# Kernel tuning notes

Measured on AMD Instinct MI355X. Metric: run time of the kernel, lower is better.

The kernel has to match this reference:

```python
import jax, jax.numpy as jnp
import numpy as np

B = 8          # batch (number of ragged segments)
N = 4096       # trigram sets per sequence (uniform segments)
K = 3          # trigram token ids per set
V = 100000     # vocab_size
H = 1024       # hidden_size
SEQ = 2048     # sequence_length / seq_len


def setup_inputs() -> dict:
    key = jax.random.key(0)
    k1, k2 = jax.random.split(key)
    trigram_token_ids = jax.random.randint(k1, (B * N, K), 0, V, dtype=jnp.int32)
    # each position covered by exactly 2 trigram sets; per-segment positions start at 0
    pos_one = (jnp.arange(N, dtype=jnp.int32) // 2)  # [N], values 0..SEQ-1
    trigram_set_position_ids = jnp.tile(pos_one, B)  # [B*N]
    starts = jnp.arange(B, dtype=jnp.int32) * N
    trigram_token_ids_offsets = jnp.stack([starts, starts + N], axis=1)  # [B,2]
    std = (2.0 / (5.0 * H)) ** 0.5  # pythia init
    W = jax.random.normal(k2, (V, H), dtype=jnp.float32) * std
    return {
        "trigram_set_position_ids": trigram_set_position_ids,
        "trigram_token_ids": trigram_token_ids,
        "trigram_token_ids_offsets": trigram_token_ids_offsets,
        "seq_len": SEQ,
        "W": W,
    }


def reference(trigram_set_position_ids, trigram_token_ids, trigram_token_ids_offsets, seq_len, W):
    # Uniform ragged segments: reshape flat arrays to [B, n, ...] using offsets count.
    b = trigram_token_ids_offsets.shape[0]
    total, k = trigram_token_ids.shape
    n = total // b
    tok = trigram_token_ids.reshape(b, n, k)          # [B, n, K]
    pos = trigram_set_position_ids.reshape(b, n)      # [B, n]
    # gather + mean-aggregate over the K trigram ids of each set
    emb = W[tok].mean(axis=2)                         # [B, n, H]

    def scatter_one(p, e):
        # index_add scatter of set embeddings onto sequence positions
        s = jax.ops.segment_sum(e, p, num_segments=seq_len)                       # [seq, H]
        c = jax.ops.segment_sum(jnp.ones((n,), e.dtype), p, num_segments=seq_len)  # [seq]
        c = jnp.where(c == 0, jnp.ones((), e.dtype), c)  # counts of 0 -> 1 (normalization guard)
        return s / c[:, None]

    return jax.vmap(scatter_one)(pos, emb)            # [B, seq, H]
```

## Files before the change

### kernel.cpp

```cpp
#include <hip/hip_runtime.h>

#define CAP 8
#define RPB 16

__global__ void build_map_kernel(const int* __restrict__ pos_ids,
                                 const int* __restrict__ tok,
                                 int total, int n_per, int seq, int K,
                                 int* __restrict__ counts,
                                 int* __restrict__ toktab) {
    int i = blockIdx.x * blockDim.x + threadIdx.x;
    if (i >= total) return;
    int b = i / n_per;
    int p = pos_ids[i];
    if ((unsigned)p >= (unsigned)seq) return;
    int bp = b * seq + p;
    int c = atomicAdd(&counts[bp], 1);
    if (c < CAP) {
        int* dst = toktab + (size_t)bp * (CAP * K) + c * K;
        for (int k = 0; k < K; ++k) dst[k] = tok[i * K + k];
    }
}

#define SORT2(a, b) { int _lo = min(a, b); int _hi = max(a, b); a = _lo; b = _hi; }

__global__ void sort_rows_kernel(const int* __restrict__ counts,
                                 int* __restrict__ toktab,
                                 int nrows, int K) {
    int i = blockIdx.x * blockDim.x + threadIdx.x;
    if (i >= nrows) return;
    int cnt = counts[i];
    int ce = cnt < CAP ? cnt : CAP;
    int n = ce * K;
    int stride = CAP * K;
    int* row = toktab + (size_t)i * stride;
    if (n == 6) {
        int t0=row[0],t1=row[1],t2=row[2],t3=row[3],t4=row[4],t5=row[5];
        SORT2(t1,t2) SORT2(t4,t5) SORT2(t0,t2) SORT2(t3,t5)
        SORT2(t0,t1) SORT2(t3,t4) SORT2(t1,t4) SORT2(t0,t3)
        SORT2(t2,t5) SORT2(t1,t3) SORT2(t2,t4) SORT2(t2,t3)
        row[0]=t0;row[1]=t1;row[2]=t2;row[3]=t3;row[4]=t4;row[5]=t5;
    } else if (n > 1) {
        int tmp[CAP * 8];
        if (n > CAP * 8) n = CAP * 8;
        for (int j = 0; j < n; ++j) tmp[j] = row[j];
        for (int a = 1; a < n; ++a) {
            int v = tmp[a]; int q = a - 1;
            while (q >= 0 && tmp[q] > v) { tmp[q + 1] = tmp[q]; --q; }
            tmp[q + 1] = v;
        }
        for (int j = 0; j < n; ++j) row[j] = tmp[j];
    }
}

__global__ __launch_bounds__(256, 4)
void gather_out_kernel(const float* __restrict__ W,
                       const int* __restrict__ counts,
                       const int* __restrict__ toktab,
                       float* __restrict__ out,
                       int K, int H, int nrows) {
    int r0 = blockIdx.x * RPB;
    int h = threadIdx.x * 4;
    int stride = CAP * K;

    int cnt[RPB];
    bool allsix = true;
    #pragma unroll
    for (int r = 0; r < RPB; ++r) {
        int row = r0 + r;
        cnt[r] = (row < nrows) ? counts[row] : 0;
        int ce = cnt[r] < CAP ? cnt[r] : CAP;
        if (ce * K != 6) allsix = false;
    }

    float4 acc[RPB];
    #pragma unroll
    for (int r = 0; r < RPB; ++r) acc[r] = make_float4(0.f, 0.f, 0.f, 0.f);

    if (allsix) {
        #pragma unroll
        for (int j = 0; j < 6; ++j) {
            #pragma unroll
            for (int r = 0; r < RPB; ++r) {
                int t = toktab[(size_t)(r0 + r) * stride + j];
                const float4 v = *(const float4*)(W + (size_t)t * H + h);
                acc[r].x += v.x; acc[r].y += v.y;
                acc[r].z += v.z; acc[r].w += v.w;
            }
        }
    } else {
        #pragma unroll
        for (int r = 0; r < RPB; ++r) {
            int ce = cnt[r] < CAP ? cnt[r] : CAP;
            int ntok = ce * K;
            for (int j = 0; j < ntok; ++j) {
                int t = toktab[(size_t)(r0 + r) * stride + j];
                const float4 v = *(const float4*)(W + (size_t)t * H + h);
                acc[r].x += v.x; acc[r].y += v.y;
                acc[r].z += v.z; acc[r].w += v.w;
            }
        }
    }

    #pragma unroll
    for (int r = 0; r < RPB; ++r) {
        int row = r0 + r;
        if (row >= nrows) continue;
        float denom = (float)K * (float)(cnt[r] > 0 ? cnt[r] : 1);
        float s = 1.0f / denom;
        float* op = out + (size_t)row * H + h;
        __builtin_nontemporal_store(acc[r].x * s, op + 0);
        __builtin_nontemporal_store(acc[r].y * s, op + 1);
        __builtin_nontemporal_store(acc[r].z * s, op + 2);
        __builtin_nontemporal_store(acc[r].w * s, op + 3);
    }
}

extern "C" void kernel_launch(void* const* d_in, const int* in_sizes, int n_in,
                              void* d_out, int out_size, void* d_ws, size_t ws_size,
                              hipStream_t stream) {
    const int*   pos_ids = (const int*)d_in[0];
    const int*   tok     = (const int*)d_in[1];
    const float* W       = (const float*)d_in[4];
    float*       out     = (float*)d_out;

    const int B     = in_sizes[2] / 2;
    const int total = in_sizes[0];
    const int n_per = total / B;
    const int K     = in_sizes[1] / total;
    const int H     = 1024;
    const int seq   = out_size / (B * H);
    const int nrows = B * seq;

    int* counts = (int*)d_ws;
    int* toktab = counts + (size_t)nrows;

    hipMemsetAsync(counts, 0, (size_t)nrows * sizeof(int), stream);

    int bthreads = 256;
    int bblocks  = (total + bthreads - 1) / bthreads;
    build_map_kernel<<<bblocks, bthreads, 0, stream>>>(pos_ids, tok, total,
                                                       n_per, seq, K,
                                                       counts, toktab);

    int sblocks = (nrows + bthreads - 1) / bthreads;
    sort_rows_kernel<<<sblocks, bthreads, 0, stream>>>(counts, toktab,
                                                       nrows, K);

    int gblocks = (nrows + RPB - 1) / RPB;
    gather_out_kernel<<<gblocks, H / 4, 0, stream>>>(W, counts, toktab,
                                                     out, K, H, nrows);
}
```

Measured before the change: 88.82 us.

## Fold row sort into gather and split vocab gathers into barrier-synced phases

Removes the separate sort kernel by sorting each row's token ids in shared memory inside the gather kernel. The gather is then split into two vocab-range phases separated by a grid-wide soft barrier, so that all blocks touch the same half of W at once and it is more likely to stay in cache. The barrier gives up after a spin limit, so correctness does not depend on it, but blocks that finish early may sleep-wait. It also adds a per-token range check and shared-memory indexing inside the hot loop.

After: 244.6 us. 2.75x slower.

```diff
diff --git a/kernel.cpp b/kernel.cpp
--- a/kernel.cpp
+++ b/kernel.cpp
@@ -1,7 +1,10 @@
 #include <hip/hip_runtime.h>
 
 #define CAP 8
+#define MAXT (CAP * 3)
 #define RPB 16
+#define NPHASE 2
+#define SPIN_LIMIT 2000
 
 __global__ void build_map_kernel(const int* __restrict__ pos_ids,
                                  const int* __restrict__ tok,
@@ -23,89 +26,92 @@
 
 #define SORT2(a, b) { int _lo = min(a, b); int _hi = max(a, b); a = _lo; b = _hi; }
 
-__global__ void sort_rows_kernel(const int* __restrict__ counts,
-                                 int* __restrict__ toktab,
-                                 int nrows, int K) {
-    int i = blockIdx.x * blockDim.x + threadIdx.x;
-    if (i >= nrows) return;
-    int cnt = counts[i];
-    int ce = cnt < CAP ? cnt : CAP;
-    int n = ce * K;
-    int stride = CAP * K;
-    int* row = toktab + (size_t)i * stride;
-    if (n == 6) {
-        int t0=row[0],t1=row[1],t2=row[2],t3=row[3],t4=row[4],t5=row[5];
-        SORT2(t1,t2) SORT2(t4,t5) SORT2(t0,t2) SORT2(t3,t5)
-        SORT2(t0,t1) SORT2(t3,t4) SORT2(t1,t4) SORT2(t0,t3)
-        SORT2(t2,t5) SORT2(t1,t3) SORT2(t2,t4) SORT2(t2,t3)
-        row[0]=t0;row[1]=t1;row[2]=t2;row[3]=t3;row[4]=t4;row[5]=t5;
-    } else if (n > 1) {
-        int tmp[CAP * 8];
-        if (n > CAP * 8) n = CAP * 8;
-        for (int j = 0; j < n; ++j) tmp[j] = row[j];
-        for (int a = 1; a < n; ++a) {
-            int v = tmp[a]; int q = a - 1;
-            while (q >= 0 && tmp[q] > v) { tmp[q + 1] = tmp[q]; --q; }
-            tmp[q + 1] = v;
+__device__ void soft_barrier(int* ctr, int target) {
+    __syncthreads();
+    if (threadIdx.x == 0) {
+        __hip_atomic_fetch_add(ctr, 1, __ATOMIC_ACQ_REL, __HIP_MEMORY_SCOPE_AGENT);
+        int spins = 0;
+        while (__hip_atomic_load(ctr, __ATOMIC_ACQUIRE,
+                                 __HIP_MEMORY_SCOPE_AGENT) < target) {
+            if (++spins > SPIN_LIMIT) break;
+            __builtin_amdgcn_s_sleep(16);
         }
-        for (int j = 0; j < n; ++j) row[j] = tmp[j];
     }
+    __syncthreads();
 }
 
 __global__ __launch_bounds__(256, 4)
-void gather_out_kernel(const float* __restrict__ W,
-                       const int* __restrict__ counts,
-                       const int* __restrict__ toktab,
-                       float* __restrict__ out,
-                       int K, int H, int nrows) {
+void gather_phase_kernel(const float* __restrict__ W,
+                         const int* __restrict__ counts,
+                         const int* __restrict__ toktab,
+                         float* __restrict__ out,
+                         int* __restrict__ bar,
+                         int K, int H, int nrows, int V, int nblocks) {
     int r0 = blockIdx.x * RPB;
     int h = threadIdx.x * 4;
     int stride = CAP * K;
 
-    int cnt[RPB];
-    bool allsix = true;
-    #pragma unroll
-    for (int r = 0; r < RPB; ++r) {
+    __shared__ int s_tok[RPB][MAXT];
+    __shared__ int s_cnt[RPB];
+    __shared__ int s_ntok[RPB];
+
+    if (threadIdx.x < RPB) {
+        int r = threadIdx.x;
         int row = r0 + r;
-        cnt[r] = (row < nrows) ? counts[row] : 0;
-        int ce = cnt[r] < CAP ? cnt[r] : CAP;
-        if (ce * K != 6) allsix = false;
+        int cnt = (row < nrows) ? counts[row] : 0;
+        int ce = cnt < CAP ? cnt : CAP;
+        int n = ce * K; if (n > MAXT) n = MAXT;
+        s_cnt[r] = cnt;
+        s_ntok[r] = n;
+        const int* tp = toktab + (size_t)row * stride;
+        if (n == 6) {
+            int t0=tp[0],t1=tp[1],t2=tp[2],t3=tp[3],t4=tp[4],t5=tp[5];
+            SORT2(t1,t2) SORT2(t4,t5) SORT2(t0,t2) SORT2(t3,t5)
+            SORT2(t0,t1) SORT2(t3,t4) SORT2(t1,t4) SORT2(t0,t3)
+            SORT2(t2,t5) SORT2(t1,t3) SORT2(t2,t4) SORT2(t2,t3)
+            s_tok[r][0]=t0; s_tok[r][1]=t1; s_tok[r][2]=t2;
+            s_tok[r][3]=t3; s_tok[r][4]=t4; s_tok[r][5]=t5;
+        } else if (n > 0) {
+            for (int j = 0; j < n; ++j) s_tok[r][j] = tp[j];
+            for (int a = 1; a < n; ++a) {
+                int v = s_tok[r][a]; int q = a - 1;
+                while (q >= 0 && s_tok[r][q] > v) {
+                    s_tok[r][q + 1] = s_tok[r][q]; --q;
+                }
+                s_tok[r][q + 1] = v;
+            }
+        }
     }
+    __syncthreads();
 
     float4 acc[RPB];
     #pragma unroll
     for (int r = 0; r < RPB; ++r) acc[r] = make_float4(0.f, 0.f, 0.f, 0.f);
 
-    if (allsix) {
+    for (int ph = 0; ph < NPHASE; ++ph) {
+        int lo = (int)(((long long)ph * V) / NPHASE);
+        int hi = (int)(((long long)(ph + 1) * V) / NPHASE);
         #pragma unroll
-        for (int j = 0; j < 6; ++j) {
-            #pragma unroll
-            for (int r = 0; r < RPB; ++r) {
-                int t = toktab[(size_t)(r0 + r) * stride + j];
-                const float4 v = *(const float4*)(W + (size_t)t * H + h);
-                acc[r].x += v.x; acc[r].y += v.y;
-                acc[r].z += v.z; acc[r].w += v.w;
+        for (int r = 0; r < RPB; ++r) {
+            int n = s_ntok[r];
+            for (int j = 0; j < n; ++j) {
+                int t = s_tok[r][j];
+                if (t >= lo && t < hi) {
+                    const float4 v = *(const float4*)(W + (size_t)t * H + h);
+                    acc[r].x += v.x; acc[r].y += v.y;
+                    acc[r].z += v.z; acc[r].w += v.w;
+                }
             }
         }
-    } else {
-        #pragma unroll
-        for (int r = 0; r < RPB; ++r) {
-            int ce = cnt[r] < CAP ? cnt[r] : CAP;
-            int ntok = ce * K;
-            for (int j = 0; j < ntok; ++j) {
-                int t = toktab[(size_t)(r0 + r) * stride + j];
-                const float4 v = *(const float4*)(W + (size_t)t * H + h);
-                acc[r].x += v.x; acc[r].y += v.y;
-                acc[r].z += v.z; acc[r].w += v.w;
-            }
-        }
+        if (ph + 1 < NPHASE) soft_barrier(&bar[ph], nblocks);
     }
 
     #pragma unroll
     for (int r = 0; r < RPB; ++r) {
         int row = r0 + r;
         if (row >= nrows) continue;
-        float denom = (float)K * (float)(cnt[r] > 0 ? cnt[r] : 1);
+        int cnt = s_cnt[r];
+        float denom = (float)K * (float)(cnt > 0 ? cnt : 1);
         float s = 1.0f / denom;
         float* op = out + (size_t)row * H + h;
         __builtin_nontemporal_store(acc[r].x * s, op + 0);
@@ -130,11 +136,13 @@
     const int H     = 1024;
     const int seq   = out_size / (B * H);
     const int nrows = B * seq;
+    const int V     = in_sizes[4] / H;
 
-    int* counts = (int*)d_ws;
+    int* bar    = (int*)d_ws;
+    int* counts = bar + NPHASE;
     int* toktab = counts + (size_t)nrows;
 
-    hipMemsetAsync(counts, 0, (size_t)nrows * sizeof(int), stream);
+    hipMemsetAsync(bar, 0, (size_t)(NPHASE + nrows) * sizeof(int), stream);
 
     int bthreads = 256;
     int bblocks  = (total + bthreads - 1) / bthreads;
@@ -142,11 +150,8 @@
                                                        n_per, seq, K,
                                                        counts, toktab);
 
-    int sblocks = (nrows + bthreads - 1) / bthreads;
-    sort_rows_kernel<<<sblocks, bthreads, 0, stream>>>(counts, toktab,
-                                                       nrows, K);
-
     int gblocks = (nrows + RPB - 1) / RPB;
-    gather_out_kernel<<<gblocks, H / 4, 0, stream>>>(W, counts, toktab,
-                                                     out, K, H, nrows);
+    gather_phase_kernel<<<gblocks, H / 4, 0, stream>>>(W, counts, toktab,
+                                                       out, bar, K, H,
+                                                       nrows, V, gblocks);
 }
```
